# Optimization experiments

Measured on AMD Instinct MI355X. Metric: run time of the kernel, lower is better.

## Reference

```python
import jax, jax.numpy as jnp
import numpy as np


def setup_inputs() -> dict:
    key = jax.random.key(0)
    kq, kk, kv, km = jax.random.split(key, 4)
    B, H, N, D = 2, 16, 2048, 64
    q = jax.random.normal(kq, (B, H, N, D), dtype=jnp.float32)
    k = jax.random.normal(kk, (B, H, N, D), dtype=jnp.float32)
    v = jax.random.normal(kv, (B, H, N, D), dtype=jnp.float32)
    # mask > 0 (True) means the key position is masked OUT (matches masked_fill semantics)
    mask = jax.random.randint(km, (B, N), 0, 2).astype(bool)
    return {"q": q, "k": k, "v": v, "mask": mask}


def reference(q, k, v, mask):
    # q, k, v: [b, h, n, d]; mask: [b, n] (True = masked out)
    scale = q.shape[-1] ** -0.5
    sim = jnp.einsum('bhid,bhjd->bhij', q, k) * scale
    # L2-distance score: 2*q.k - |q|^2 - |k|^2 (scaled dot already includes `scale`)
    q_sq = jnp.sum(q ** 2, axis=-1, keepdims=True)            # [b, h, n, 1]
    k_sq = jnp.sum(k ** 2, axis=-1, keepdims=True).swapaxes(-1, -2)  # [b, h, 1, n]
    sim = sim * 2 - q_sq - k_sq
    neg_max = -jnp.finfo(sim.dtype).max
    sim = jnp.where(mask[:, None, None, :], neg_max, sim)
    attn = jax.nn.softmax(sim, axis=-1)
    out = jnp.einsum('bhij,bhjd->bhid', attn, v)
    return out
```

## Files before the change

### kernel.cpp

```cpp
#include <hip/hip_runtime.h>

#define B_ 2
#define H_ 16
#define N_ 2048
#define D_ 64
#define NH_ (B_*H_)
#define ROWS_ (NH_*N_)
#define KVB 64
#define NT (N_/KVB)
#define LOG2E 1.4426950408889634f
#define QSCALE (0.25f * LOG2E)

typedef _Float16 f16;
typedef _Float16 f16x4 __attribute__((ext_vector_type(4)));
typedef _Float16 f16x8 __attribute__((ext_vector_type(8)));
typedef float f32x4 __attribute__((ext_vector_type(4)));

typedef __attribute__((address_space(1))) const void g_void;
typedef __attribute__((address_space(3))) void l_void;

__device__ __forceinline__ void gl_lds16(const void* g, void* l) {
  __builtin_amdgcn_global_load_lds((g_void*)g, (l_void*)l, 16, 0, 0);
}

__global__ __launch_bounds__(256) void prep_all(
    const float* __restrict__ q, const float* __restrict__ k,
    const float* __restrict__ v, const void* __restrict__ mask,
    f16* __restrict__ qh, f16* __restrict__ kh, f16* __restrict__ vt,
    float* __restrict__ bias) {
  int tid = threadIdx.x;
  if (blockIdx.x < 1024) {
    int head = blockIdx.x >> 5;
    int n0 = (blockIdx.x & 31) << 6;
    int e = tid & 15, gq = tid >> 4;
    const float* src = v + ((long)head * N_ + n0 + e * 4) * D_ + gq * 4;
    f32x4 r0 = *(const f32x4*)(src);
    f32x4 r1 = *(const f32x4*)(src + D_);
    f32x4 r2 = *(const f32x4*)(src + 2 * D_);
    f32x4 r3 = *(const f32x4*)(src + 3 * D_);
    f16* dst = vt + (long)head * D_ * N_ + n0 + e * 4;
#pragma unroll
    for (int c = 0; c < 4; ++c) {
      f16x4 y;
      y[0] = (f16)r0[c]; y[1] = (f16)r1[c]; y[2] = (f16)r2[c]; y[3] = (f16)r3[c];
      *(f16x4*)(dst + (long)(gq * 4 + c) * N_) = y;
    }
  } else {
    int wid = (blockIdx.x - 1024) * 4 + (tid >> 6);
    int lane = tid & 63;
    int r8 = lane >> 3, e = lane & 7;
    const unsigned* mw = (const unsigned*)mask;
    bool bytes_mode = __any(mw[lane] > 1u);
#pragma unroll
    for (int trip = 0; trip < 4; ++trip) {
      long grow = ((long)(trip * 4096 + wid)) * 8 + r8;
      bool isK = grow >= ROWS_;
      long row = isK ? grow - ROWS_ : grow;
      const float* s = (isK ? k : q) + row * D_ + e * 8;
      f32x4 x0 = *(const f32x4*)s;
      f32x4 x1 = *(const f32x4*)(s + 4);
      float scl = isK ? 1.0f : QSCALE;
      f16x8 hv;
#pragma unroll
      for (int c = 0; c < 4; ++c) { hv[c] = (f16)(x0[c] * scl); hv[4 + c] = (f16)(x1[c] * scl); }
      *(f16x8*)((isK ? kh : qh) + row * D_ + e * 8) = hv;
      if (isK) {
        float sq = x0[0]*x0[0] + x0[1]*x0[1] + x0[2]*x0[2] + x0[3]*x0[3]
                 + x1[0]*x1[0] + x1[1]*x1[1] + x1[2]*x1[2] + x1[3]*x1[3];
        sq += __shfl_xor(sq, 1); sq += __shfl_xor(sq, 2); sq += __shfl_xor(sq, 4);
        if (e == 0) {
          int b = (int)(row >> 15);
          int n = (int)(row & (N_ - 1));
          int mv = bytes_mode ? (int)((const unsigned char*)mask)[b * N_ + n]
                              : ((const int*)mask)[b * N_ + n];
          bias[row] = mv ? -1e30f : -sq * LOG2E;
        }
      }
    }
  }
}

__global__ __launch_bounds__(256, 4) void attend_main(
    const f16* __restrict__ qh, const f16* __restrict__ kh,
    const f16* __restrict__ vt, const float* __restrict__ bias,
    float* __restrict__ out) {
  __shared__ f16 Kt[2][4096];
  __shared__ f16 Vt[2][4096];
  __shared__ f16 Pb[4][1024];

  int tid = threadIdx.x;
  int w = tid >> 6, lane = tid & 63;
  int j = lane & 15, g = lane >> 4;

  int bid = (blockIdx.x & 7) * 128 + (blockIdx.x >> 3);
  int head = bid >> 5;
  int qt = bid & 31;
  int qrow0 = qt * 64 + w * 16;

  const f16* qbase = qh + ((long)head * N_ + qrow0 + j) * D_;
  f16x8 qf0 = *(const f16x8*)(qbase + g * 8);
  f16x8 qf1 = *(const f16x8*)(qbase + 32 + g * 8);

  const char* kg = (const char*)(kh + (long)head * N_ * D_);
  const char* vg = (const char*)(vt + (long)head * D_ * N_);
  const float* bb = bias + (long)head * N_ + g * 4;

  f32x4 O0 = {0.f,0.f,0.f,0.f}, O1 = {0.f,0.f,0.f,0.f};
  f32x4 O2 = {0.f,0.f,0.f,0.f}, O3 = {0.f,0.f,0.f,0.f};
  float m = -1e30f, l = 0.f;

  auto stage = [&](int buf, int t) {
    int kv = t * KVB;
    if (w < 2) {
      const char* src = kg + (size_t)kv * 128;
      char* lb = (char*)&Kt[buf][0];
#pragma unroll
      for (int c = 0; c < 4; ++c) {
        int chunk = w * 4 + c;
        int o = chunk * 1024 + lane * 16;
        int p = o ^ (((o >> 7) & 7) << 4);
        gl_lds16(src + p, lb + chunk * 1024);
      }
    } else {
      const char* src = vg + (size_t)kv * 2;
      char* lb = (char*)&Vt[buf][0];
#pragma unroll
      for (int c = 0; c < 4; ++c) {
        int chunk = (w - 2) * 4 + c;
        int o = chunk * 1024 + lane * 16;
        int p = o ^ (((o >> 7) & 7) << 4);
        gl_lds16(src + (size_t)(p >> 7) * (N_ * 2) + (p & 127), lb + chunk * 1024);
      }
    }
  };

  f32x4 bnx[4];
#pragma unroll
  for (int jt = 0; jt < 4; ++jt) bnx[jt] = *(const f32x4*)(bb + jt * 16);

  stage(0, 0);
  __syncthreads();
  int cur = 0;

  for (int t = 0; t < NT; ++t) {
    f32x4 sA[4];
#pragma unroll
    for (int jt = 0; jt < 4; ++jt) sA[jt] = bnx[jt];
    if (t + 1 < NT) {
      stage(cur ^ 1, t + 1);
#pragma unroll
      for (int jt = 0; jt < 4; ++jt)
        bnx[jt] = *(const f32x4*)(bb + (t + 1) * KVB + jt * 16);
    }

    const char* Kc = (const char*)&Kt[cur][0];
    const char* Vc = (const char*)&Vt[cur][0];

    __builtin_amdgcn_s_setprio(1);
#pragma unroll
    for (int jt = 0; jt < 4; ++jt) {
      int r = jt * 16 + j;
      int base = r << 7;
      int sw = (r & 7) << 4;
      f16x8 k0 = *(const f16x8*)(Kc + ((base + g * 16) ^ sw));
      f16x8 k1 = *(const f16x8*)(Kc + ((base + 64 + g * 16) ^ sw));
      sA[jt] = __builtin_amdgcn_mfma_f32_16x16x32_f16(k0, qf0, sA[jt], 0, 0, 0);
      sA[jt] = __builtin_amdgcn_mfma_f32_16x16x32_f16(k1, qf1, sA[jt], 0, 0, 0);
    }
    __builtin_amdgcn_s_setprio(0);

    f32x4 mx0, mx1;
#pragma unroll
    for (int r = 0; r < 4; ++r) { mx0[r] = fmaxf(sA[0][r], sA[1][r]); mx1[r] = fmaxf(sA[2][r], sA[3][r]); }
    float tm = -1e30f;
#pragma unroll
    for (int r = 0; r < 4; ++r) tm = fmaxf(tm, fmaxf(mx0[r], mx1[r]));
    tm = fmaxf(tm, __shfl_xor(tm, 16));
    tm = fmaxf(tm, __shfl_xor(tm, 32));
    float mn = fmaxf(m, tm);
    float sc = __builtin_amdgcn_exp2f(m - mn);
    m = mn;

    float rsum = 0.f;
#pragma unroll
    for (int jt = 0; jt < 4; ++jt)
#pragma unroll
      for (int r = 0; r < 4; ++r) {
        float p = __builtin_amdgcn_exp2f(sA[jt][r] - mn);
        sA[jt][r] = p;
        rsum += p;
      }
    rsum += __shfl_xor(rsum, 16);
    rsum += __shfl_xor(rsum, 32);
    l = l * sc + rsum;

#pragma unroll
    for (int r = 0; r < 4; ++r) {
      float scr = __shfl(sc, g * 4 + r);
      O0[r] *= scr; O1[r] *= scr; O2[r] *= scr; O3[r] *= scr;
    }

    char* Pw = (char*)&Pb[w][0];
#pragma unroll
    for (int jt = 0; jt < 4; ++jt) {
      f16x4 pk;
      pk[0] = (f16)sA[jt][0]; pk[1] = (f16)sA[jt][1];
      pk[2] = (f16)sA[jt][2]; pk[3] = (f16)sA[jt][3];
      int off = ((j << 7) + jt * 32 + g * 8) ^ ((j & 7) << 4);
      *(f16x4*)(Pw + off) = pk;
    }
    int swp = (j & 7) << 4;
    f16x8 pf0 = *(const f16x8*)(Pw + (((j << 7) + g * 16) ^ swp));
    f16x8 pf1 = *(const f16x8*)(Pw + (((j << 7) + 64 + g * 16) ^ swp));

    __builtin_amdgcn_s_setprio(1);
#pragma unroll
    for (int dt = 0; dt < 4; ++dt) {
      int row = dt * 16 + j;
      int base = row << 7;
      int sw = (row & 7) << 4;
      f16x8 v0 = *(const f16x8*)(Vc + ((base + g * 16) ^ sw));
      f16x8 v1 = *(const f16x8*)(Vc + ((base + 64 + g * 16) ^ sw));
      f32x4* Od = (dt == 0) ? &O0 : (dt == 1) ? &O1 : (dt == 2) ? &O2 : &O3;
      *Od = __builtin_amdgcn_mfma_f32_16x16x32_f16(pf0, v0, *Od, 0, 0, 0);
      *Od = __builtin_amdgcn_mfma_f32_16x16x32_f16(pf1, v1, *Od, 0, 0, 0);
    }
    __builtin_amdgcn_s_setprio(0);

    __syncthreads();
    cur ^= 1;
  }

  float* ob = out + ((long)head * N_ + qrow0 + g * 4) * D_ + j;
#pragma unroll
  for (int r = 0; r < 4; ++r) {
    float inv = 1.0f / __shfl(l, g * 4 + r);
    float* o2 = ob + (long)r * D_;
    o2[0]  = O0[r] * inv;
    o2[16] = O1[r] * inv;
    o2[32] = O2[r] * inv;
    o2[48] = O3[r] * inv;
  }
}

extern "C" void kernel_launch(void* const* d_in, const int* in_sizes, int n_in,
                              void* d_out, int out_size, void* d_ws, size_t ws_size,
                              hipStream_t stream) {
  const float* q = (const float*)d_in[0];
  const float* k = (const float*)d_in[1];
  const float* v = (const float*)d_in[2];
  const void* mask = d_in[3];

  char* ws = (char*)d_ws;
  f16*   qh   = (f16*)ws;
  f16*   kh   = (f16*)(ws + (8u  << 20));
  f16*   vt   = (f16*)(ws + (16u << 20));
  float* bias = (float*)(ws + (24u << 20));
  float* out  = (float*)d_out;

  prep_all<<<dim3(2048), dim3(256), 0, stream>>>(q, k, v, mask, qh, kh, vt, bias);
  attend_main<<<dim3(NH_ * (N_ / 64)), dim3(256), 0, stream>>>(qh, kh, vt, bias, out);
}
```

Measured before the change: 161.8 us.

## Add lazy softmax rescale, stagger KV start per block, precompute LDS offsets

Result: faster. 155.0 us (-4.2%).

```diff
diff --git a/kernel.cpp b/kernel.cpp
--- a/kernel.cpp
+++ b/kernel.cpp
@@ -96,6 +96,7 @@
   int head = bid >> 5;
   int qt = bid & 31;
   int qrow0 = qt * 64 + w * 16;
+  int off = ((bid >> 5) & 3) * 8;
 
   const f16* qbase = qh + ((long)head * N_ + qrow0 + j) * D_;
   f16x8 qf0 = *(const f16x8*)(qbase + g * 8);
@@ -104,6 +105,19 @@
   const char* kg = (const char*)(kh + (long)head * N_ * D_);
   const char* vg = (const char*)(vt + (long)head * D_ * N_);
   const float* bb = bias + (long)head * N_ + g * 4;
+
+  int ko0[4], ko1[4];
+#pragma unroll
+  for (int x = 0; x < 4; ++x) {
+    int rk = x * 16 + j;
+    int swk = (rk & 7) << 4;
+    ko0[x] = ((rk << 7) + g * 16) ^ swk;
+    ko1[x] = ((rk << 7) + 64 + g * 16) ^ swk;
+  }
+  int pswz = (j & 7) << 4;
+  int pw0 = ((j << 7) + g * 8) ^ pswz;
+  int pr0 = ((j << 7) + g * 16) ^ pswz;
+  int pr1 = ((j << 7) + 64 + g * 16) ^ pswz;
 
   f32x4 O0 = {0.f,0.f,0.f,0.f}, O1 = {0.f,0.f,0.f,0.f};
   f32x4 O2 = {0.f,0.f,0.f,0.f}, O3 = {0.f,0.f,0.f,0.f};
@@ -136,21 +150,23 @@
 
   f32x4 bnx[4];
 #pragma unroll
-  for (int jt = 0; jt < 4; ++jt) bnx[jt] = *(const f32x4*)(bb + jt * 16);
-
-  stage(0, 0);
+  for (int jt = 0; jt < 4; ++jt) bnx[jt] = *(const f32x4*)(bb + off * KVB + jt * 16);
+
+  stage(0, off);
   __syncthreads();
   int cur = 0;
 
   for (int t = 0; t < NT; ++t) {
+    int tt = (t + off) & (NT - 1);
     f32x4 sA[4];
 #pragma unroll
     for (int jt = 0; jt < 4; ++jt) sA[jt] = bnx[jt];
     if (t + 1 < NT) {
-      stage(cur ^ 1, t + 1);
+      int tn = (tt + 1) & (NT - 1);
+      stage(cur ^ 1, tn);
 #pragma unroll
       for (int jt = 0; jt < 4; ++jt)
-        bnx[jt] = *(const f32x4*)(bb + (t + 1) * KVB + jt * 16);
+        bnx[jt] = *(const f32x4*)(bb + tn * KVB + jt * 16);
     }
 
     const char* Kc = (const char*)&Kt[cur][0];
@@ -159,11 +175,8 @@
     __builtin_amdgcn_s_setprio(1);
 #pragma unroll
     for (int jt = 0; jt < 4; ++jt) {
-      int r = jt * 16 + j;
-      int base = r << 7;
-      int sw = (r & 7) << 4;
-      f16x8 k0 = *(const f16x8*)(Kc + ((base + g * 16) ^ sw));
-      f16x8 k1 = *(const f16x8*)(Kc + ((base + 64 + g * 16) ^ sw));
+      f16x8 k0 = *(const f16x8*)(Kc + ko0[jt]);
+      f16x8 k1 = *(const f16x8*)(Kc + ko1[jt]);
       sA[jt] = __builtin_amdgcn_mfma_f32_16x16x32_f16(k0, qf0, sA[jt], 0, 0, 0);
       sA[jt] = __builtin_amdgcn_mfma_f32_16x16x32_f16(k1, qf1, sA[jt], 0, 0, 0);
     }
@@ -177,28 +190,32 @@
     for (int r = 0; r < 4; ++r) tm = fmaxf(tm, fmaxf(mx0[r], mx1[r]));
     tm = fmaxf(tm, __shfl_xor(tm, 16));
     tm = fmaxf(tm, __shfl_xor(tm, 32));
-    float mn = fmaxf(m, tm);
-    float sc = __builtin_amdgcn_exp2f(m - mn);
-    m = mn;
+
+    bool fastok = (tm - m <= 8.0f) && (m > -1e29f);
+    if (!__all(fastok)) {
+      float mn = fmaxf(m, tm);
+      float sc = __builtin_amdgcn_exp2f(m - mn);
+      m = mn;
+      l *= sc;
+#pragma unroll
+      for (int r = 0; r < 4; ++r) {
+        float scr = __shfl(sc, g * 4 + r);
+        O0[r] *= scr; O1[r] *= scr; O2[r] *= scr; O3[r] *= scr;
+      }
+    }
 
     float rsum = 0.f;
 #pragma unroll
     for (int jt = 0; jt < 4; ++jt)
 #pragma unroll
       for (int r = 0; r < 4; ++r) {
-        float p = __builtin_amdgcn_exp2f(sA[jt][r] - mn);
+        float p = __builtin_amdgcn_exp2f(sA[jt][r] - m);
         sA[jt][r] = p;
         rsum += p;
       }
     rsum += __shfl_xor(rsum, 16);
     rsum += __shfl_xor(rsum, 32);
-    l = l * sc + rsum;
-
-#pragma unroll
-    for (int r = 0; r < 4; ++r) {
-      float scr = __shfl(sc, g * 4 + r);
-      O0[r] *= scr; O1[r] *= scr; O2[r] *= scr; O3[r] *= scr;
-    }
+    l += rsum;
 
     char* Pw = (char*)&Pb[w][0];
 #pragma unroll
@@ -206,21 +223,16 @@
       f16x4 pk;
       pk[0] = (f16)sA[jt][0]; pk[1] = (f16)sA[jt][1];
       pk[2] = (f16)sA[jt][2]; pk[3] = (f16)sA[jt][3];
-      int off = ((j << 7) + jt * 32 + g * 8) ^ ((j & 7) << 4);
-      *(f16x4*)(Pw + off) = pk;
-    }
-    int swp = (j & 7) << 4;
-    f16x8 pf0 = *(const f16x8*)(Pw + (((j << 7) + g * 16) ^ swp));
-    f16x8 pf1 = *(const f16x8*)(Pw + (((j << 7) + 64 + g * 16) ^ swp));
+      *(f16x4*)(Pw + (pw0 ^ (jt * 32))) = pk;
+    }
+    f16x8 pf0 = *(const f16x8*)(Pw + pr0);
+    f16x8 pf1 = *(const f16x8*)(Pw + pr1);
 
     __builtin_amdgcn_s_setprio(1);
 #pragma unroll
     for (int dt = 0; dt < 4; ++dt) {
-      int row = dt * 16 + j;
-      int base = row << 7;
-      int sw = (row & 7) << 4;
-      f16x8 v0 = *(const f16x8*)(Vc + ((base + g * 16) ^ sw));
-      f16x8 v1 = *(const f16x8*)(Vc + ((base + 64 + g * 16) ^ sw));
+      f16x8 v0 = *(const f16x8*)(Vc + ko0[dt]);
+      f16x8 v1 = *(const f16x8*)(Vc + ko1[dt]);
       f32x4* Od = (dt == 0) ? &O0 : (dt == 1) ? &O1 : (dt == 2) ? &O2 : &O3;
       *Od = __builtin_amdgcn_mfma_f32_16x16x32_f16(pf0, v0, *Od, 0, 0, 0);
       *Od = __builtin_amdgcn_mfma_f32_16x16x32_f16(pf1, v1, *Od, 0, 0, 0);
```
